# Optimization experiments

Measured on AMD Instinct MI355X. Metric: run time of the kernel, lower is better.

Reference implementation:

```python
import jax, jax.numpy as jnp
import numpy as np

N, D = 8192, 32
SIGMA = 4.0
DAMPING = 0.5
MAX_ITER = 10
SHIFT_TOL = 1e-4


def _sqdist(a, b):
    # squared euclidean distances, (Na, Nb)
    sq = jnp.sum(a * a, axis=1)[:, None] + jnp.sum(b * b, axis=1)[None, :] - 2.0 * (a @ b.T)
    return jnp.maximum(sq, 0.0)


def setup_inputs() -> dict:
    key = jax.random.key(0)
    x = jax.random.normal(key, (N, D), dtype=jnp.float32)
    sigma = jnp.asarray(SIGMA, dtype=jnp.float32)  # learned scalar nn.Parameter
    return {"x": x, "sigma": sigma}


def _find_centroids(x, sigma):
    gamma = 1.0 / (2.0 * sigma ** 2)

    def body(carry, _):
        centroids, done = carry
        sq = _sqdist(x, centroids)              # (N, N); cdist(x,c)**2
        w = jnp.exp(-sq * gamma)                # gaussian kernel weights
        new_c = (w @ x) / jnp.sum(w, axis=1, keepdims=True)
        shift = jnp.linalg.norm(new_c - centroids, axis=1)
        # torch breaks BEFORE the damping update when max shift < tol
        done_new = done | (jnp.max(shift) < SHIFT_TOL)
        centroids = jnp.where(done_new, centroids,
                              DAMPING * centroids + (1.0 - DAMPING) * new_c)
        return (centroids, done_new), None

    (centroids, _), _ = jax.lax.scan(jax.remat(body), (x, jnp.asarray(False)), None, length=MAX_ITER)
    return centroids


def _nms_keep(x, centroids, threshold):
    n = centroids.shape[0]
    sq_pc = _sqdist(x, centroids)
    closest = jnp.argmin(sq_pc, axis=1)                      # (N,)
    scores = jnp.zeros((n,), jnp.int32).at[closest].add(1)   # counts per centroid
    sq_cc = _sqdist(centroids, centroids)
    overlap = (sq_cc < threshold ** 2) & ~jnp.eye(n, dtype=bool)
    order = jnp.argsort(-scores)                             # descending by score

    def body(keep, idx):
        active = keep[idx]
        keep2 = jnp.where(active, keep & ~overlap[idx], keep)
        keep2 = keep2.at[idx].set(jnp.where(active, scores[idx] > 0, keep2[idx]))
        return keep2, None

    keep, _ = jax.lax.scan(body, jnp.ones((n,), bool), order)
    return keep


def reference(x, sigma):
    centroids = _find_centroids(x, sigma)
    # threshold = sigma.item() in torch -> constant w.r.t. autodiff
    keep = _nms_keep(x, centroids, jax.lax.stop_gradient(sigma))
    # assignment over kept centroids only (dropped centroids get -inf cost -> 0 prob)
    cost = -jnp.sqrt(_sqdist(x, centroids) + 1e-12)
    cost = jnp.where(keep[None, :], cost, -jnp.inf)
    assignment = jax.nn.softmax(cost, axis=1)  # alpha == 1 branch
    return centroids, assignment, keep
```

## Files before the change

kernel.cpp:

```cpp
#include <hip/hip_runtime.h>
#include <math.h>

#define NPTS 8192
#define DIM 32
#define MAX_ITER 10
#define TOL 1e-4f
#define DAMP 0.5f

#define OFF_MSP   0u
#define OFF_CCUR  8650752u
#define OFF_CNEW  8912896u
#define OFF_NX    9175040u
#define OFF_NC    9183232u
#define OFF_PV    9191424u
#define OFF_PJ    9453568u
#define OFF_RKP   9715712u
#define OFF_PM    9977856u
#define OFF_PS   10240000u
#define OFF_MSH  10502144u
#define OFF_SCO  10502208u
#define OFF_ORD  10510400u

__global__ __launch_bounds__(256) void k_init(const float* __restrict__ x,
                                              float* __restrict__ c0,
                                              float* __restrict__ nx,
                                              float* __restrict__ nc) {
    int p = blockIdx.x * blockDim.x + threadIdx.x;
    const float4* xr = (const float4*)(x + (size_t)p * DIM);
    float4* cr = (float4*)(c0 + (size_t)p * DIM);
    float s = 0.f;
#pragma unroll
    for (int q = 0; q < 8; ++q) {
        float4 v = xr[q];
        cr[q] = v;
        s += v.x * v.x + v.y * v.y + v.z * v.z + v.w * v.w;
    }
    nx[p] = s;
    nc[p] = s;
}

__global__ __launch_bounds__(256) void k_ms2(const float* __restrict__ x,
                                             const float* __restrict__ nx,
                                             const float* __restrict__ c,
                                             const float* __restrict__ nc,
                                             const float* __restrict__ sigma_p,
                                             float* __restrict__ P) {
    int t = threadIdx.x;
    int wv = __builtin_amdgcn_readfirstlane(t >> 6);
    int lane = t & 63;
    int it = (int)blockIdx.x >> 5, js = (int)blockIdx.x & 31;
    int i = it * 256 + wv * 64 + lane;

    float sg = sigma_p[0];
    float gamma = 1.f / (2.f * sg * sg);

    float xi[DIM];
    const float4* xr = (const float4*)(x + (size_t)i * DIM);
#pragma unroll
    for (int q = 0; q < 8; ++q) {
        float4 v = xr[q];
        xi[4 * q] = v.x; xi[4 * q + 1] = v.y; xi[4 * q + 2] = v.z; xi[4 * q + 3] = v.w;
    }
    float nxi = nx[i];

    float acc[DIM];
#pragma unroll
    for (int d = 0; d < DIM; ++d) acc[d] = 0.f;
    float wsum = 0.f;

    int j0 = js * 256;
    const float* cb = c + (size_t)j0 * DIM;
    const float* xb = x + (size_t)j0 * DIM;
    const float* ncb = nc + j0;

    for (int jj = 0; jj < 256; ++jj) {
        const float4* cr = (const float4*)(cb + (size_t)jj * DIM);
        const float4* xr2 = (const float4*)(xb + (size_t)jj * DIM);
        float4 C[8], X[8];
#pragma unroll
        for (int q = 0; q < 8; ++q) C[q] = cr[q];
#pragma unroll
        for (int q = 0; q < 8; ++q) X[q] = xr2[q];
        float ncj = ncb[jj];
        float d0 = 0.f, d1 = 0.f, d2 = 0.f, d3 = 0.f;
#pragma unroll
        for (int q = 0; q < 8; ++q) {
            d0 = fmaf(xi[4 * q + 0], C[q].x, d0);
            d1 = fmaf(xi[4 * q + 1], C[q].y, d1);
            d2 = fmaf(xi[4 * q + 2], C[q].z, d2);
            d3 = fmaf(xi[4 * q + 3], C[q].w, d3);
        }
        float sq = fmaxf(nxi + ncj - 2.f * ((d0 + d1) + (d2 + d3)), 0.f);
        float w = __expf(-sq * gamma);
        wsum += w;
#pragma unroll
        for (int q = 0; q < 8; ++q) {
            acc[4 * q + 0] = fmaf(w, X[q].x, acc[4 * q + 0]);
            acc[4 * q + 1] = fmaf(w, X[q].y, acc[4 * q + 1]);
            acc[4 * q + 2] = fmaf(w, X[q].z, acc[4 * q + 2]);
            acc[4 * q + 3] = fmaf(w, X[q].w, acc[4 * q + 3]);
        }
    }

    size_t base = ((size_t)js * 33) * NPTS + i;
#pragma unroll
    for (int d = 0; d < DIM; ++d) P[base + (size_t)d * NPTS] = acc[d];
    P[base + (size_t)32 * NPTS] = wsum;
}

__global__ __launch_bounds__(256) void k_reduce(const float* __restrict__ P,
                                                const float* __restrict__ c_cur,
                                                float* __restrict__ c_new,
                                                unsigned int* __restrict__ maxshift) {
    int i = blockIdx.x * 256 + threadIdx.x;
    float tot[33];
#pragma unroll
    for (int d = 0; d < 33; ++d) tot[d] = 0.f;
    for (int js = 0; js < 32; ++js) {
        size_t base = ((size_t)js * 33) * NPTS + i;
#pragma unroll
        for (int d = 0; d < 33; ++d) tot[d] += P[base + (size_t)d * NPTS];
    }
    float ws = tot[32];
    const float* co = c_cur + (size_t)i * DIM;
    float sh2 = 0.f;
    float ncv[DIM];
#pragma unroll
    for (int d = 0; d < DIM; ++d) {
        float v = tot[d] / ws;
        ncv[d] = v;
        float df = v - co[d];
        sh2 = fmaf(df, df, sh2);
    }
    float4* dst = (float4*)(c_new + (size_t)i * DIM);
#pragma unroll
    for (int q = 0; q < 8; ++q)
        dst[q] = make_float4(ncv[4 * q], ncv[4 * q + 1], ncv[4 * q + 2], ncv[4 * q + 3]);
    atomicMax(maxshift, __float_as_uint(sqrtf(sh2)));
}

__global__ __launch_bounds__(256) void k_update(float* __restrict__ c_cur,
                                                const float* __restrict__ c_new,
                                                float* __restrict__ nc,
                                                const unsigned int* __restrict__ maxshift) {
    if (__uint_as_float(*maxshift) < TOL) return;
    int i = blockIdx.x * 256 + threadIdx.x;
    float4* cc = (float4*)(c_cur + (size_t)i * DIM);
    const float4* cn = (const float4*)(c_new + (size_t)i * DIM);
    float s = 0.f;
#pragma unroll
    for (int q = 0; q < 8; ++q) {
        float4 a = cc[q], b = cn[q];
        float4 r = make_float4(DAMP * a.x + (1.f - DAMP) * b.x,
                               DAMP * a.y + (1.f - DAMP) * b.y,
                               DAMP * a.z + (1.f - DAMP) * b.z,
                               DAMP * a.w + (1.f - DAMP) * b.w);
        cc[q] = r;
        s += r.x * r.x + r.y * r.y + r.z * r.z + r.w * r.w;
    }
    nc[i] = s;
}

__global__ __launch_bounds__(256) void k_scores2(const float* __restrict__ x,
                                                 const float* __restrict__ nx,
                                                 const float* __restrict__ c,
                                                 const float* __restrict__ nc,
                                                 float* __restrict__ pv,
                                                 int* __restrict__ pj) {
    int t = threadIdx.x;
    int wv = __builtin_amdgcn_readfirstlane(t >> 6);
    int lane = t & 63;
    int it = (int)blockIdx.x >> 5, js = (int)blockIdx.x & 31;
    int p = it * 256 + wv * 64 + lane;

    float xi[DIM];
    const float4* xr = (const float4*)(x + (size_t)p * DIM);
#pragma unroll
    for (int q = 0; q < 8; ++q) {
        float4 v = xr[q];
        xi[4 * q] = v.x; xi[4 * q + 1] = v.y; xi[4 * q + 2] = v.z; xi[4 * q + 3] = v.w;
    }
    float nxp = nx[p];

    int j0 = js * 256;
    const float* cb = c + (size_t)j0 * DIM;
    const float* ncb = nc + j0;
    float bestv = INFINITY;
    int bestj = j0;
    for (int jj = 0; jj < 256; ++jj) {
        const float4* cr = (const float4*)(cb + (size_t)jj * DIM);
        float4 C[8];
#pragma unroll
        for (int q = 0; q < 8; ++q) C[q] = cr[q];
        float d0 = 0.f, d1 = 0.f, d2 = 0.f, d3 = 0.f;
#pragma unroll
        for (int q = 0; q < 8; ++q) {
            d0 = fmaf(xi[4 * q + 0], C[q].x, d0);
            d1 = fmaf(xi[4 * q + 1], C[q].y, d1);
            d2 = fmaf(xi[4 * q + 2], C[q].z, d2);
            d3 = fmaf(xi[4 * q + 3], C[q].w, d3);
        }
        float sq = fmaxf(nxp + ncb[jj] - 2.f * ((d0 + d1) + (d2 + d3)), 0.f);
        if (sq < bestv) { bestv = sq; bestj = j0 + jj; }
    }
    pv[(size_t)js * NPTS + p] = bestv;
    pj[(size_t)js * NPTS + p] = bestj;
}

__global__ __launch_bounds__(256) void k_score_comb(const float* __restrict__ pv,
                                                    const int* __restrict__ pj,
                                                    int* __restrict__ scores) {
    int p = blockIdx.x * 256 + threadIdx.x;
    float bv = pv[p];
    int bj = pj[p];
    for (int js = 1; js < 32; ++js) {
        float v = pv[(size_t)js * NPTS + p];
        int j = pj[(size_t)js * NPTS + p];
        if (v < bv) { bv = v; bj = j; }
    }
    atomicAdd(&scores[bj], 1);
}

__global__ __launch_bounds__(256) void k_rank_part(const int* __restrict__ scores,
                                                   int* __restrict__ rkp) {
    int t = threadIdx.x;
    int wv = __builtin_amdgcn_readfirstlane(t >> 6);
    int lane = t & 63;
    int it = (int)blockIdx.x >> 5, js = (int)blockIdx.x & 31;
    int p = it * 256 + wv * 64 + lane;
    int sp = scores[p];
    int j0 = js * 256;
    int r = 0;
    for (int jj = 0; jj < 256; ++jj) {
        int sj = scores[j0 + jj];
        int j = j0 + jj;
        r += (sj > sp) || (sj == sp && j < p);
    }
    rkp[(size_t)js * NPTS + p] = r;
}

__global__ __launch_bounds__(256) void k_rank_comb(const int* __restrict__ rkp,
                                                   int* __restrict__ order) {
    int p = blockIdx.x * 256 + threadIdx.x;
    int r = 0;
    for (int js = 0; js < 32; ++js) r += rkp[(size_t)js * NPTS + p];
    order[r] = p;
}

__global__ __launch_bounds__(1024) void k_nms(const float* __restrict__ c,
                                              const int* __restrict__ order,
                                              const int* __restrict__ scores,
                                              const float* __restrict__ sigma_p,
                                              float* __restrict__ keep_out) {
    __shared__ int s_ord[NPTS];
    __shared__ unsigned char kp[NPTS];
    __shared__ int s_first[16];
    __shared__ int s_next;
    int t = threadIdx.x;
    for (int q = t; q < NPTS; q += 1024) { s_ord[q] = order[q]; kp[q] = 1; }
    __syncthreads();
    float sg = sigma_p[0];
    float thr2 = sg * sg;

    int k = 0;
    while (k < NPTS) {
        int cand = k + t;
        bool hit = (cand < NPTS) && (kp[s_ord[cand]] != 0);
        unsigned long long b = __ballot(hit);
        int wave = t >> 6;
        if ((t & 63) == 0)
            s_first[wave] = b ? (k + (wave << 6) + (__ffsll((unsigned long long)b) - 1))
                              : 0x7fffffff;
        __syncthreads();
        if (t == 0) {
            int mn = s_first[0];
            for (int w2 = 1; w2 < 16; ++w2) mn = min(mn, s_first[w2]);
            s_next = mn;
        }
        __syncthreads();
        int kf = s_next;
        if (kf == 0x7fffffff) { k += 1024; continue; }

        int idx = s_ord[kf];
        float ci[DIM];
        const float4* cr = (const float4*)(c + (size_t)idx * DIM);
#pragma unroll
        for (int q = 0; q < 8; ++q) {
            float4 v = cr[q];
            ci[4 * q] = v.x; ci[4 * q + 1] = v.y; ci[4 * q + 2] = v.z; ci[4 * q + 3] = v.w;
        }
#pragma unroll
        for (int m2 = 0; m2 < 8; ++m2) {
            int j = t + m2 * 1024;
            const float4* cj = (const float4*)(c + (size_t)j * DIM);
            float sq = 0.f;
#pragma unroll
            for (int q = 0; q < 8; ++q) {
                float4 v = cj[q];
                float e0 = v.x - ci[4 * q], e1 = v.y - ci[4 * q + 1];
                float e2 = v.z - ci[4 * q + 2], e3 = v.w - ci[4 * q + 3];
                sq += e0 * e0 + e1 * e1 + e2 * e2 + e3 * e3;
            }
            if (j != idx && sq < thr2) kp[j] = 0;
        }
        __syncthreads();
        if (t == 0) kp[idx] = (scores[idx] > 0) ? 1 : 0;
        __syncthreads();
        k = kf + 1;
    }
    __syncthreads();
    for (int q = t; q < NPTS; q += 1024) keep_out[q] = kp[q] ? 1.0f : 0.0f;
}

__global__ __launch_bounds__(256) void k_apass1(const float* __restrict__ x,
                                                const float* __restrict__ nx,
                                                const float* __restrict__ c,
                                                const float* __restrict__ nc,
                                                const float* __restrict__ keepf,
                                                float* __restrict__ pm,
                                                float* __restrict__ ps) {
    int t = threadIdx.x;
    int wv = __builtin_amdgcn_readfirstlane(t >> 6);
    int lane = t & 63;
    int it = (int)blockIdx.x >> 5, js = (int)blockIdx.x & 31;
    int p = it * 256 + wv * 64 + lane;

    float xi[DIM];
    const float4* xr = (const float4*)(x + (size_t)p * DIM);
#pragma unroll
    for (int q = 0; q < 8; ++q) {
        float4 v = xr[q];
        xi[4 * q] = v.x; xi[4 * q + 1] = v.y; xi[4 * q + 2] = v.z; xi[4 * q + 3] = v.w;
    }
    float nxp = nx[p];

    int j0 = js * 256;
    const float* cb = c + (size_t)j0 * DIM;
    const float* ncb = nc + j0;
    const float* kb = keepf + j0;
    float m = -1e30f, S = 0.f;
    for (int jj = 0; jj < 256; ++jj) {
        const float4* cr = (const float4*)(cb + (size_t)jj * DIM);
        float4 C[8];
#pragma unroll
        for (int q = 0; q < 8; ++q) C[q] = cr[q];
        float d0 = 0.f, d1 = 0.f, d2 = 0.f, d3 = 0.f;
#pragma unroll
        for (int q = 0; q < 8; ++q) {
            d0 = fmaf(xi[4 * q + 0], C[q].x, d0);
            d1 = fmaf(xi[4 * q + 1], C[q].y, d1);
            d2 = fmaf(xi[4 * q + 2], C[q].z, d2);
            d3 = fmaf(xi[4 * q + 3], C[q].w, d3);
        }
        float sq = fmaxf(nxp + ncb[jj] - 2.f * ((d0 + d1) + (d2 + d3)), 0.f);
        float cost = -sqrtf(sq + 1e-12f);
        float ck = (kb[jj] > 0.5f) ? cost : -INFINITY;
        float mn = fmaxf(m, ck);
        S = S * __expf(m - mn) + __expf(ck - mn);
        m = mn;
    }
    pm[(size_t)js * NPTS + p] = m;
    ps[(size_t)js * NPTS + p] = S;
}

__global__ __launch_bounds__(256) void k_acomb(const float* __restrict__ pm,
                                               const float* __restrict__ ps,
                                               const float* __restrict__ nx,
                                               float* __restrict__ A) {
    int p = blockIdx.x * 256 + threadIdx.x;
    float M = -1e30f;
    for (int js = 0; js < 32; ++js) M = fmaxf(M, pm[(size_t)js * NPTS + p]);
    float SS = 0.f;
    for (int js = 0; js < 32; ++js)
        SS += ps[(size_t)js * NPTS + p] * __expf(pm[(size_t)js * NPTS + p] - M);
    float* row = A + (size_t)p * NPTS;
    row[8189] = nx[p];
    row[8190] = M;
    row[8191] = 1.f / SS;
}

__global__ __launch_bounds__(256) void k_apass2(const float* __restrict__ x,
                                                const float* __restrict__ c,
                                                const float* __restrict__ keepf,
                                                float* __restrict__ A) {
    __shared__ float sNX[16], sM[16], sI[16];
    int t = threadIdx.x;
    int wv = __builtin_amdgcn_readfirstlane(t >> 6);
    int lane = t & 63;
    int p0 = blockIdx.x * 16;
    if (t < 16) {
        const float* row = A + (size_t)(p0 + t) * NPTS;
        sNX[t] = row[8189];
        sM[t] = row[8190];
        sI[t] = row[8191];
    }
    __syncthreads();

    for (int ch = wv; ch < 128; ch += 4) {
        int j = ch * 64 + lane;
        float cj[DIM];
        const float4* cr = (const float4*)(c + (size_t)j * DIM);
        float ncj = 0.f;
#pragma unroll
        for (int q = 0; q < 8; ++q) {
            float4 v = cr[q];
            cj[4 * q] = v.x; cj[4 * q + 1] = v.y; cj[4 * q + 2] = v.z; cj[4 * q + 3] = v.w;
            ncj += v.x * v.x + v.y * v.y + v.z * v.z + v.w * v.w;
        }
        float kpj = keepf[j];
        for (int pp = 0; pp < 16; ++pp) {
            const float4* xrow = (const float4*)(x + (size_t)(p0 + pp) * DIM);
            float4 X[8];
#pragma unroll
            for (int q = 0; q < 8; ++q) X[q] = xrow[q];
            float nxp = sNX[pp], M = sM[pp], inv = sI[pp];
            float d0 = 0.f, d1 = 0.f, d2 = 0.f, d3 = 0.f;
#pragma unroll
            for (int q = 0; q < 8; ++q) {
                d0 = fmaf(cj[4 * q + 0], X[q].x, d0);
                d1 = fmaf(cj[4 * q + 1], X[q].y, d1);
                d2 = fmaf(cj[4 * q + 2], X[q].z, d2);
                d3 = fmaf(cj[4 * q + 3], X[q].w, d3);
            }
            float sq = fmaxf(nxp + ncj - 2.f * ((d0 + d1) + (d2 + d3)), 0.f);
            float cost = -sqrtf(sq + 1e-12f);
            float v = (kpj > 0.5f) ? __expf(cost - M) * inv : 0.f;
            A[(size_t)(p0 + pp) * NPTS + j] = v;
        }
    }
}

extern "C" void kernel_launch(void* const* d_in, const int* in_sizes, int n_in,
                              void* d_out, int out_size, void* d_ws, size_t ws_size,
                              hipStream_t stream) {
    const float* x = (const float*)d_in[0];
    const float* sigma = (const float*)d_in[1];

    float* out = (float*)d_out;
    float* OUT_C = out;
    float* A = out + (size_t)NPTS * DIM;
    float* OUT_K = A + (size_t)NPTS * NPTS;

    float* msP = A + OFF_MSP;
    float* c_cur = A + OFF_CCUR;
    float* c_new = A + OFF_CNEW;
    float* nx = A + OFF_NX;
    float* nc = A + OFF_NC;
    float* pv = A + OFF_PV;
    int* pj = (int*)(A + OFF_PJ);
    int* rkp = (int*)(A + OFF_RKP);
    float* pm = A + OFF_PM;
    float* ps = A + OFF_PS;
    unsigned int* maxshift = (unsigned int*)(A + OFF_MSH);
    int* scores = (int*)(A + OFF_SCO);
    int* order = (int*)(A + OFF_ORD);

    k_init<<<NPTS / 256, 256, 0, stream>>>(x, c_cur, nx, nc);
    for (int itr = 0; itr < MAX_ITER; ++itr) {
        hipMemsetAsync(maxshift, 0, sizeof(unsigned int), stream);
        k_ms2<<<1024, 256, 0, stream>>>(x, nx, c_cur, nc, sigma, msP);
        k_reduce<<<NPTS / 256, 256, 0, stream>>>(msP, c_cur, c_new, maxshift);
        k_update<<<NPTS / 256, 256, 0, stream>>>(c_cur, c_new, nc, maxshift);
    }
    hipMemcpyAsync(OUT_C, c_cur, (size_t)NPTS * DIM * sizeof(float),
                   hipMemcpyDeviceToDevice, stream);

    hipMemsetAsync(scores, 0, NPTS * sizeof(int), stream);
    k_scores2<<<1024, 256, 0, stream>>>(x, nx, OUT_C, nc, pv, pj);
    k_score_comb<<<NPTS / 256, 256, 0, stream>>>(pv, pj, scores);
    k_rank_part<<<1024, 256, 0, stream>>>(scores, rkp);
    k_rank_comb<<<NPTS / 256, 256, 0, stream>>>(rkp, order);
    k_nms<<<1, 1024, 0, stream>>>(OUT_C, order, scores, sigma, OUT_K);

    k_apass1<<<1024, 256, 0, stream>>>(x, nx, OUT_C, nc, OUT_K, pm, ps);
    k_acomb<<<NPTS / 256, 256, 0, stream>>>(pm, ps, nx, A);
    k_apass2<<<NPTS / 16, 256, 0, stream>>>(x, OUT_C, OUT_K, A);
}
```

Measured before the change: 1.888 ms.

## Interleave centroids, x and norms into one padded row buffer; drop softmax max pass

Packs the current centroid, the original x row, the centroid norm and the keep flag into a single 68-float padded row, so the mean-shift, argmin and softmax passes stream one contiguous buffer. The separate memsets are folded into the init kernel, and each iteration gets its own max-shift slot. The softmax max-tracking and combine kernel are removed, since the costs are at most zero, and exp2/rcp/sqrt intrinsics are used instead. The assignment write pass is re-tiled to 128 points by 512 centroids with two centroids per thread. This risks reduced precision from the fast intrinsics and from dropping max-subtraction, and it relies on the workspace for the partial sums.

```diff
diff --git a/kernel.cpp b/kernel.cpp
--- a/kernel.cpp
+++ b/kernel.cpp
@@ -6,110 +6,110 @@
 #define MAX_ITER 10
 #define TOL 1e-4f
 #define DAMP 0.5f
-
-#define OFF_MSP   0u
-#define OFF_CCUR  8650752u
-#define OFF_CNEW  8912896u
-#define OFF_NX    9175040u
-#define OFF_NC    9183232u
-#define OFF_PV    9191424u
-#define OFF_PJ    9453568u
-#define OFF_RKP   9715712u
-#define OFF_PM    9977856u
-#define OFF_PS   10240000u
-#define OFF_MSH  10502144u
-#define OFF_SCO  10502208u
-#define OFF_ORD  10510400u
+#define LOG2E 1.4426950408889634f
+#define CXS 68
+
+#define OFF_MSP    0u
+#define OFF_CXF    8650752u
+#define OFF_CNEW   9207808u
+#define OFF_NX     9469952u
+#define OFF_PV     9478144u
+#define OFF_PJ     9740288u
+#define OFF_RKP   10002432u
+#define OFF_MSH   10264576u
+#define OFF_SCO   10264592u
+#define OFF_ORD   10272784u
 
 __global__ __launch_bounds__(256) void k_init(const float* __restrict__ x,
-                                              float* __restrict__ c0,
+                                              float* __restrict__ cxf,
                                               float* __restrict__ nx,
-                                              float* __restrict__ nc) {
+                                              int* __restrict__ scores,
+                                              unsigned int* __restrict__ msh) {
     int p = blockIdx.x * blockDim.x + threadIdx.x;
     const float4* xr = (const float4*)(x + (size_t)p * DIM);
-    float4* cr = (float4*)(c0 + (size_t)p * DIM);
+    float* row = cxf + (size_t)p * CXS;
     float s = 0.f;
 #pragma unroll
     for (int q = 0; q < 8; ++q) {
         float4 v = xr[q];
-        cr[q] = v;
+        ((float4*)row)[q] = v;
+        ((float4*)row)[8 + q] = v;
         s += v.x * v.x + v.y * v.y + v.z * v.z + v.w * v.w;
     }
+    row[64] = s;
+    row[65] = 0.f;
     nx[p] = s;
-    nc[p] = s;
+    scores[p] = 0;
+    if (blockIdx.x == 0 && threadIdx.x < 16) msh[threadIdx.x] = 0u;
 }
 
 __global__ __launch_bounds__(256) void k_ms2(const float* __restrict__ x,
                                              const float* __restrict__ nx,
-                                             const float* __restrict__ c,
-                                             const float* __restrict__ nc,
+                                             const float* __restrict__ cxf,
                                              const float* __restrict__ sigma_p,
                                              float* __restrict__ P) {
     int t = threadIdx.x;
-    int wv = __builtin_amdgcn_readfirstlane(t >> 6);
-    int lane = t & 63;
     int it = (int)blockIdx.x >> 5, js = (int)blockIdx.x & 31;
-    int i = it * 256 + wv * 64 + lane;
+    int i = it * 256 + t;
+    int jb = js * 256;
 
     float sg = sigma_p[0];
-    float gamma = 1.f / (2.f * sg * sg);
+    float ng2 = -LOG2E / (2.f * sg * sg);
 
     float xi[DIM];
-    const float4* xr = (const float4*)(x + (size_t)i * DIM);
-#pragma unroll
-    for (int q = 0; q < 8; ++q) {
-        float4 v = xr[q];
-        xi[4 * q] = v.x; xi[4 * q + 1] = v.y; xi[4 * q + 2] = v.z; xi[4 * q + 3] = v.w;
+    {
+        const float4* xr = (const float4*)(x + (size_t)i * DIM);
+#pragma unroll
+        for (int q = 0; q < 8; ++q) {
+            float4 a = xr[q];
+            xi[4 * q] = a.x; xi[4 * q + 1] = a.y; xi[4 * q + 2] = a.z; xi[4 * q + 3] = a.w;
+        }
     }
     float nxi = nx[i];
 
     float acc[DIM];
 #pragma unroll
     for (int d = 0; d < DIM; ++d) acc[d] = 0.f;
-    float wsum = 0.f;
-
-    int j0 = js * 256;
-    const float* cb = c + (size_t)j0 * DIM;
-    const float* xb = x + (size_t)j0 * DIM;
-    const float* ncb = nc + j0;
+    float ws = 0.f;
+
+    const float* row = cxf + (size_t)jb * CXS;
 
     for (int jj = 0; jj < 256; ++jj) {
-        const float4* cr = (const float4*)(cb + (size_t)jj * DIM);
-        const float4* xr2 = (const float4*)(xb + (size_t)jj * DIM);
-        float4 C[8], X[8];
-#pragma unroll
-        for (int q = 0; q < 8; ++q) C[q] = cr[q];
-#pragma unroll
-        for (int q = 0; q < 8; ++q) X[q] = xr2[q];
-        float ncj = ncb[jj];
-        float d0 = 0.f, d1 = 0.f, d2 = 0.f, d3 = 0.f;
-#pragma unroll
-        for (int q = 0; q < 8; ++q) {
-            d0 = fmaf(xi[4 * q + 0], C[q].x, d0);
-            d1 = fmaf(xi[4 * q + 1], C[q].y, d1);
-            d2 = fmaf(xi[4 * q + 2], C[q].z, d2);
-            d3 = fmaf(xi[4 * q + 3], C[q].w, d3);
-        }
-        float sq = fmaxf(nxi + ncj - 2.f * ((d0 + d1) + (d2 + d3)), 0.f);
-        float w = __expf(-sq * gamma);
-        wsum += w;
-#pragma unroll
-        for (int q = 0; q < 8; ++q) {
-            acc[4 * q + 0] = fmaf(w, X[q].x, acc[4 * q + 0]);
-            acc[4 * q + 1] = fmaf(w, X[q].y, acc[4 * q + 1]);
-            acc[4 * q + 2] = fmaf(w, X[q].z, acc[4 * q + 2]);
-            acc[4 * q + 3] = fmaf(w, X[q].w, acc[4 * q + 3]);
-        }
+        float w;
+        {
+            float a0 = 0.f, a1 = 0.f, a2 = 0.f, a3 = 0.f;
+#pragma unroll
+            for (int q = 0; q < 8; ++q) {
+                float4 cv = ((const float4*)row)[q];
+                a0 = fmaf(xi[4 * q + 0], cv.x, a0);
+                a1 = fmaf(xi[4 * q + 1], cv.y, a1);
+                a2 = fmaf(xi[4 * q + 2], cv.z, a2);
+                a3 = fmaf(xi[4 * q + 3], cv.w, a3);
+            }
+            float ncj = row[64];
+            float sq = fmaxf(fmaf(-2.f, (a0 + a1) + (a2 + a3), nxi + ncj), 0.f);
+            w = __builtin_amdgcn_exp2f(ng2 * sq);
+        }
+        ws += w;
+#pragma unroll
+        for (int q = 0; q < 8; ++q) {
+            float4 xv = ((const float4*)row)[8 + q];
+            acc[4 * q + 0] = fmaf(w, xv.x, acc[4 * q + 0]);
+            acc[4 * q + 1] = fmaf(w, xv.y, acc[4 * q + 1]);
+            acc[4 * q + 2] = fmaf(w, xv.z, acc[4 * q + 2]);
+            acc[4 * q + 3] = fmaf(w, xv.w, acc[4 * q + 3]);
+        }
+        row += CXS;
     }
 
     size_t base = ((size_t)js * 33) * NPTS + i;
 #pragma unroll
     for (int d = 0; d < DIM; ++d) P[base + (size_t)d * NPTS] = acc[d];
-    P[base + (size_t)32 * NPTS] = wsum;
+    P[base + (size_t)32 * NPTS] = ws;
 }
 
 __global__ __launch_bounds__(256) void k_reduce(const float* __restrict__ P,
-                                                const float* __restrict__ c_cur,
+                                                const float* __restrict__ cxf,
                                                 float* __restrict__ c_new,
                                                 unsigned int* __restrict__ maxshift) {
     int i = blockIdx.x * 256 + threadIdx.x;
@@ -122,12 +122,14 @@
         for (int d = 0; d < 33; ++d) tot[d] += P[base + (size_t)d * NPTS];
     }
     float ws = tot[32];
-    const float* co = c_cur + (size_t)i * DIM;
+    float inv = __builtin_amdgcn_rcpf(ws);
+    inv = inv * (2.f - ws * inv);
+    const float* co = cxf + (size_t)i * CXS;
     float sh2 = 0.f;
     float ncv[DIM];
 #pragma unroll
     for (int d = 0; d < DIM; ++d) {
-        float v = tot[d] / ws;
+        float v = tot[d] * inv;
         ncv[d] = v;
         float df = v - co[d];
         sh2 = fmaf(df, df, sh2);
@@ -136,75 +138,79 @@
 #pragma unroll
     for (int q = 0; q < 8; ++q)
         dst[q] = make_float4(ncv[4 * q], ncv[4 * q + 1], ncv[4 * q + 2], ncv[4 * q + 3]);
-    atomicMax(maxshift, __float_as_uint(sqrtf(sh2)));
-}
-
-__global__ __launch_bounds__(256) void k_update(float* __restrict__ c_cur,
+    atomicMax(maxshift, __float_as_uint(__builtin_amdgcn_sqrtf(sh2)));
+}
+
+__global__ __launch_bounds__(256) void k_update(float* __restrict__ cxf,
                                                 const float* __restrict__ c_new,
-                                                float* __restrict__ nc,
                                                 const unsigned int* __restrict__ maxshift) {
     if (__uint_as_float(*maxshift) < TOL) return;
     int i = blockIdx.x * 256 + threadIdx.x;
-    float4* cc = (float4*)(c_cur + (size_t)i * DIM);
+    float* row = cxf + (size_t)i * CXS;
     const float4* cn = (const float4*)(c_new + (size_t)i * DIM);
     float s = 0.f;
 #pragma unroll
     for (int q = 0; q < 8; ++q) {
-        float4 a = cc[q], b = cn[q];
+        float4 a = ((float4*)row)[q], b = cn[q];
         float4 r = make_float4(DAMP * a.x + (1.f - DAMP) * b.x,
                                DAMP * a.y + (1.f - DAMP) * b.y,
                                DAMP * a.z + (1.f - DAMP) * b.z,
                                DAMP * a.w + (1.f - DAMP) * b.w);
-        cc[q] = r;
+        ((float4*)row)[q] = r;
         s += r.x * r.x + r.y * r.y + r.z * r.z + r.w * r.w;
     }
-    nc[i] = s;
+    row[64] = s;
+}
+
+__global__ __launch_bounds__(256) void k_extract(const float* __restrict__ cxf,
+                                                 float* __restrict__ outc) {
+    int g = blockIdx.x * 256 + threadIdx.x;
+    int rowi = g >> 3, q = g & 7;
+    ((float4*)(outc + (size_t)rowi * DIM))[q] =
+        ((const float4*)(cxf + (size_t)rowi * CXS))[q];
 }
 
 __global__ __launch_bounds__(256) void k_scores2(const float* __restrict__ x,
                                                  const float* __restrict__ nx,
-                                                 const float* __restrict__ c,
-                                                 const float* __restrict__ nc,
+                                                 const float* __restrict__ cxf,
                                                  float* __restrict__ pv,
                                                  int* __restrict__ pj) {
     int t = threadIdx.x;
-    int wv = __builtin_amdgcn_readfirstlane(t >> 6);
-    int lane = t & 63;
     int it = (int)blockIdx.x >> 5, js = (int)blockIdx.x & 31;
-    int p = it * 256 + wv * 64 + lane;
+    int p = it * 256 + t;
+    int jb = js * 256;
 
     float xi[DIM];
-    const float4* xr = (const float4*)(x + (size_t)p * DIM);
-#pragma unroll
-    for (int q = 0; q < 8; ++q) {
-        float4 v = xr[q];
-        xi[4 * q] = v.x; xi[4 * q + 1] = v.y; xi[4 * q + 2] = v.z; xi[4 * q + 3] = v.w;
+    {
+        const float4* xr = (const float4*)(x + (size_t)p * DIM);
+#pragma unroll
+        for (int q = 0; q < 8; ++q) {
+            float4 a = xr[q];
+            xi[4 * q] = a.x; xi[4 * q + 1] = a.y; xi[4 * q + 2] = a.z; xi[4 * q + 3] = a.w;
+        }
     }
     float nxp = nx[p];
 
-    int j0 = js * 256;
-    const float* cb = c + (size_t)j0 * DIM;
-    const float* ncb = nc + j0;
-    float bestv = INFINITY;
-    int bestj = j0;
+    const float* row = cxf + (size_t)jb * CXS;
+    float bv = INFINITY;
+    int bj = jb;
     for (int jj = 0; jj < 256; ++jj) {
-        const float4* cr = (const float4*)(cb + (size_t)jj * DIM);
-        float4 C[8];
-#pragma unroll
-        for (int q = 0; q < 8; ++q) C[q] = cr[q];
-        float d0 = 0.f, d1 = 0.f, d2 = 0.f, d3 = 0.f;
-#pragma unroll
-        for (int q = 0; q < 8; ++q) {
-            d0 = fmaf(xi[4 * q + 0], C[q].x, d0);
-            d1 = fmaf(xi[4 * q + 1], C[q].y, d1);
-            d2 = fmaf(xi[4 * q + 2], C[q].z, d2);
-            d3 = fmaf(xi[4 * q + 3], C[q].w, d3);
-        }
-        float sq = fmaxf(nxp + ncb[jj] - 2.f * ((d0 + d1) + (d2 + d3)), 0.f);
-        if (sq < bestv) { bestv = sq; bestj = j0 + jj; }
-    }
-    pv[(size_t)js * NPTS + p] = bestv;
-    pj[(size_t)js * NPTS + p] = bestj;
+        float a0 = 0.f, a1 = 0.f, a2 = 0.f, a3 = 0.f;
+#pragma unroll
+        for (int q = 0; q < 8; ++q) {
+            float4 cv = ((const float4*)row)[q];
+            a0 = fmaf(xi[4 * q + 0], cv.x, a0);
+            a1 = fmaf(xi[4 * q + 1], cv.y, a1);
+            a2 = fmaf(xi[4 * q + 2], cv.z, a2);
+            a3 = fmaf(xi[4 * q + 3], cv.w, a3);
+        }
+        float ncj = row[64];
+        float sq = fmaxf(fmaf(-2.f, (a0 + a1) + (a2 + a3), nxp + ncj), 0.f);
+        if (sq < bv) { bv = sq; bj = jb + jj; }
+        row += CXS;
+    }
+    pv[(size_t)js * NPTS + p] = bv;
+    pj[(size_t)js * NPTS + p] = bj;
 }
 
 __global__ __launch_bounds__(256) void k_score_comb(const float* __restrict__ pv,
@@ -224,10 +230,8 @@
 __global__ __launch_bounds__(256) void k_rank_part(const int* __restrict__ scores,
                                                    int* __restrict__ rkp) {
     int t = threadIdx.x;
-    int wv = __builtin_amdgcn_readfirstlane(t >> 6);
-    int lane = t & 63;
     int it = (int)blockIdx.x >> 5, js = (int)blockIdx.x & 31;
-    int p = it * 256 + wv * 64 + lane;
+    int p = it * 256 + t;
     int sp = scores[p];
     int j0 = js * 256;
     int r = 0;
@@ -251,7 +255,8 @@
                                               const int* __restrict__ order,
                                               const int* __restrict__ scores,
                                               const float* __restrict__ sigma_p,
-                                              float* __restrict__ keep_out) {
+                                              float* __restrict__ keep_out,
+                                              float* __restrict__ cxf) {
     __shared__ int s_ord[NPTS];
     __shared__ unsigned char kp[NPTS];
     __shared__ int s_first[16];
@@ -309,124 +314,129 @@
         k = kf + 1;
     }
     __syncthreads();
-    for (int q = t; q < NPTS; q += 1024) keep_out[q] = kp[q] ? 1.0f : 0.0f;
+    for (int q = t; q < NPTS; q += 1024) {
+        float kv = kp[q] ? 1.0f : 0.0f;
+        keep_out[q] = kv;
+        cxf[(size_t)q * CXS + 65] = kv;
+    }
 }
 
 __global__ __launch_bounds__(256) void k_apass1(const float* __restrict__ x,
                                                 const float* __restrict__ nx,
-                                                const float* __restrict__ c,
-                                                const float* __restrict__ nc,
-                                                const float* __restrict__ keepf,
-                                                float* __restrict__ pm,
+                                                const float* __restrict__ cxf,
                                                 float* __restrict__ ps) {
     int t = threadIdx.x;
-    int wv = __builtin_amdgcn_readfirstlane(t >> 6);
-    int lane = t & 63;
     int it = (int)blockIdx.x >> 5, js = (int)blockIdx.x & 31;
-    int p = it * 256 + wv * 64 + lane;
+    int p = it * 256 + t;
+    int jb = js * 256;
 
     float xi[DIM];
-    const float4* xr = (const float4*)(x + (size_t)p * DIM);
-#pragma unroll
-    for (int q = 0; q < 8; ++q) {
-        float4 v = xr[q];
-        xi[4 * q] = v.x; xi[4 * q + 1] = v.y; xi[4 * q + 2] = v.z; xi[4 * q + 3] = v.w;
+    {
+        const float4* xr = (const float4*)(x + (size_t)p * DIM);
+#pragma unroll
+        for (int q = 0; q < 8; ++q) {
+            float4 a = xr[q];
+            xi[4 * q] = a.x; xi[4 * q + 1] = a.y; xi[4 * q + 2] = a.z; xi[4 * q + 3] = a.w;
+        }
     }
     float nxp = nx[p];
 
-    int j0 = js * 256;
-    const float* cb = c + (size_t)j0 * DIM;
-    const float* ncb = nc + j0;
-    const float* kb = keepf + j0;
-    float m = -1e30f, S = 0.f;
+    const float* row = cxf + (size_t)jb * CXS;
+    float S = 0.f;
     for (int jj = 0; jj < 256; ++jj) {
-        const float4* cr = (const float4*)(cb + (size_t)jj * DIM);
-        float4 C[8];
-#pragma unroll
-        for (int q = 0; q < 8; ++q) C[q] = cr[q];
-        float d0 = 0.f, d1 = 0.f, d2 = 0.f, d3 = 0.f;
-#pragma unroll
-        for (int q = 0; q < 8; ++q) {
-            d0 = fmaf(xi[4 * q + 0], C[q].x, d0);
-            d1 = fmaf(xi[4 * q + 1], C[q].y, d1);
-            d2 = fmaf(xi[4 * q + 2], C[q].z, d2);
-            d3 = fmaf(xi[4 * q + 3], C[q].w, d3);
-        }
-        float sq = fmaxf(nxp + ncb[jj] - 2.f * ((d0 + d1) + (d2 + d3)), 0.f);
-        float cost = -sqrtf(sq + 1e-12f);
-        float ck = (kb[jj] > 0.5f) ? cost : -INFINITY;
-        float mn = fmaxf(m, ck);
-        S = S * __expf(m - mn) + __expf(ck - mn);
-        m = mn;
-    }
-    pm[(size_t)js * NPTS + p] = m;
+        float a0 = 0.f, a1 = 0.f, a2 = 0.f, a3 = 0.f;
+#pragma unroll
+        for (int q = 0; q < 8; ++q) {
+            float4 cv = ((const float4*)row)[q];
+            a0 = fmaf(xi[4 * q + 0], cv.x, a0);
+            a1 = fmaf(xi[4 * q + 1], cv.y, a1);
+            a2 = fmaf(xi[4 * q + 2], cv.z, a2);
+            a3 = fmaf(xi[4 * q + 3], cv.w, a3);
+        }
+        float ncj = row[64];
+        float kadd = (row[65] > 0.5f) ? 0.f : -1e38f;
+        float sq = fmaxf(fmaf(-2.f, (a0 + a1) + (a2 + a3), nxp + ncj), 0.f);
+        float r0 = __builtin_amdgcn_sqrtf(sq + 1e-12f);
+        S += __builtin_amdgcn_exp2f(fmaf(r0, -LOG2E, kadd));
+        row += CXS;
+    }
     ps[(size_t)js * NPTS + p] = S;
-}
-
-__global__ __launch_bounds__(256) void k_acomb(const float* __restrict__ pm,
-                                               const float* __restrict__ ps,
-                                               const float* __restrict__ nx,
-                                               float* __restrict__ A) {
-    int p = blockIdx.x * 256 + threadIdx.x;
-    float M = -1e30f;
-    for (int js = 0; js < 32; ++js) M = fmaxf(M, pm[(size_t)js * NPTS + p]);
-    float SS = 0.f;
-    for (int js = 0; js < 32; ++js)
-        SS += ps[(size_t)js * NPTS + p] * __expf(pm[(size_t)js * NPTS + p] - M);
-    float* row = A + (size_t)p * NPTS;
-    row[8189] = nx[p];
-    row[8190] = M;
-    row[8191] = 1.f / SS;
 }
 
 __global__ __launch_bounds__(256) void k_apass2(const float* __restrict__ x,
                                                 const float* __restrict__ c,
                                                 const float* __restrict__ keepf,
+                                                const float* __restrict__ ps,
                                                 float* __restrict__ A) {
-    __shared__ float sNX[16], sM[16], sI[16];
+    __shared__ float snx[128];
+    __shared__ float sscale[128];
     int t = threadIdx.x;
     int wv = __builtin_amdgcn_readfirstlane(t >> 6);
     int lane = t & 63;
-    int p0 = blockIdx.x * 16;
-    if (t < 16) {
-        const float* row = A + (size_t)(p0 + t) * NPTS;
-        sNX[t] = row[8189];
-        sM[t] = row[8190];
-        sI[t] = row[8191];
-    }
+    int pt = (int)blockIdx.x >> 4, jt = (int)blockIdx.x & 15;
+    int p0 = pt * 128, j0 = jt * 512;
+
+    if (t < 128) {
+        const float4* xr = (const float4*)(x + (size_t)(p0 + t) * DIM);
+        float s = 0.f;
+#pragma unroll
+        for (int q = 0; q < 8; ++q) {
+            float4 v = xr[q];
+            s += v.x * v.x + v.y * v.y + v.z * v.z + v.w * v.w;
+        }
+        snx[t] = s;
+        float SS = 0.f;
+        for (int js = 0; js < 32; ++js) SS += ps[(size_t)js * NPTS + p0 + t];
+        sscale[t] = 1.f / SS;
+    }
+
+    int ja = j0 + wv * 64 + lane;
+    int jbx = ja + 256;
+    float cj0[DIM], cj1[DIM];
+    float nc0 = 0.f, nc1 = 0.f;
+    {
+        const float4* cra = (const float4*)(c + (size_t)ja * DIM);
+        const float4* crb = (const float4*)(c + (size_t)jbx * DIM);
+#pragma unroll
+        for (int q = 0; q < 8; ++q) {
+            float4 va = cra[q], vb = crb[q];
+            cj0[4 * q] = va.x; cj0[4 * q + 1] = va.y; cj0[4 * q + 2] = va.z; cj0[4 * q + 3] = va.w;
+            cj1[4 * q] = vb.x; cj1[4 * q + 1] = vb.y; cj1[4 * q + 2] = vb.z; cj1[4 * q + 3] = vb.w;
+            nc0 += va.x * va.x + va.y * va.y + va.z * va.z + va.w * va.w;
+            nc1 += vb.x * vb.x + vb.y * vb.y + vb.z * vb.z + vb.w * vb.w;
+        }
+    }
+    float kadd0 = (keepf[ja] > 0.5f) ? 0.f : -1e38f;
+    float kadd1 = (keepf[jbx] > 0.5f) ? 0.f : -1e38f;
     __syncthreads();
 
-    for (int ch = wv; ch < 128; ch += 4) {
-        int j = ch * 64 + lane;
-        float cj[DIM];
-        const float4* cr = (const float4*)(c + (size_t)j * DIM);
-        float ncj = 0.f;
-#pragma unroll
-        for (int q = 0; q < 8; ++q) {
-            float4 v = cr[q];
-            cj[4 * q] = v.x; cj[4 * q + 1] = v.y; cj[4 * q + 2] = v.z; cj[4 * q + 3] = v.w;
-            ncj += v.x * v.x + v.y * v.y + v.z * v.z + v.w * v.w;
-        }
-        float kpj = keepf[j];
-        for (int pp = 0; pp < 16; ++pp) {
-            const float4* xrow = (const float4*)(x + (size_t)(p0 + pp) * DIM);
-            float4 X[8];
-#pragma unroll
-            for (int q = 0; q < 8; ++q) X[q] = xrow[q];
-            float nxp = sNX[pp], M = sM[pp], inv = sI[pp];
-            float d0 = 0.f, d1 = 0.f, d2 = 0.f, d3 = 0.f;
-#pragma unroll
-            for (int q = 0; q < 8; ++q) {
-                d0 = fmaf(cj[4 * q + 0], X[q].x, d0);
-                d1 = fmaf(cj[4 * q + 1], X[q].y, d1);
-                d2 = fmaf(cj[4 * q + 2], X[q].z, d2);
-                d3 = fmaf(cj[4 * q + 3], X[q].w, d3);
-            }
-            float sq = fmaxf(nxp + ncj - 2.f * ((d0 + d1) + (d2 + d3)), 0.f);
-            float cost = -sqrtf(sq + 1e-12f);
-            float v = (kpj > 0.5f) ? __expf(cost - M) * inv : 0.f;
-            A[(size_t)(p0 + pp) * NPTS + j] = v;
-        }
+    const float* xrow = x + (size_t)p0 * DIM;
+    for (int pp = 0; pp < 128; ++pp) {
+        float d0 = 0.f, d1 = 0.f, d2 = 0.f, d3 = 0.f;
+        float e0 = 0.f, e1 = 0.f, e2 = 0.f, e3 = 0.f;
+#pragma unroll
+        for (int q = 0; q < 8; ++q) {
+            float4 v = ((const float4*)xrow)[q];
+            d0 = fmaf(cj0[4 * q + 0], v.x, d0);
+            d1 = fmaf(cj0[4 * q + 1], v.y, d1);
+            d2 = fmaf(cj0[4 * q + 2], v.z, d2);
+            d3 = fmaf(cj0[4 * q + 3], v.w, d3);
+            e0 = fmaf(cj1[4 * q + 0], v.x, e0);
+            e1 = fmaf(cj1[4 * q + 1], v.y, e1);
+            e2 = fmaf(cj1[4 * q + 2], v.z, e2);
+            e3 = fmaf(cj1[4 * q + 3], v.w, e3);
+        }
+        float nxp = snx[pp], scl = sscale[pp];
+        float sqa = fmaxf(fmaf(-2.f, (d0 + d1) + (d2 + d3), nxp + nc0), 0.f);
+        float sqb = fmaxf(fmaf(-2.f, (e0 + e1) + (e2 + e3), nxp + nc1), 0.f);
+        float ra = __builtin_amdgcn_sqrtf(sqa + 1e-12f);
+        float rb = __builtin_amdgcn_sqrtf(sqb + 1e-12f);
+        float ta = fmaf(ra, -LOG2E, kadd0);
+        float tb = fmaf(rb, -LOG2E, kadd1);
+        float* rowp = A + (size_t)(p0 + pp) * NPTS;
+        rowp[ja] = __builtin_amdgcn_exp2f(ta) * scl;
+        rowp[jbx] = __builtin_amdgcn_exp2f(tb) * scl;
+        xrow += DIM;
     }
 }
 
@@ -442,37 +452,31 @@
     float* OUT_K = A + (size_t)NPTS * NPTS;
 
     float* msP = A + OFF_MSP;
-    float* c_cur = A + OFF_CCUR;
+    float* cxf = A + OFF_CXF;
     float* c_new = A + OFF_CNEW;
     float* nx = A + OFF_NX;
-    float* nc = A + OFF_NC;
     float* pv = A + OFF_PV;
     int* pj = (int*)(A + OFF_PJ);
     int* rkp = (int*)(A + OFF_RKP);
-    float* pm = A + OFF_PM;
-    float* ps = A + OFF_PS;
-    unsigned int* maxshift = (unsigned int*)(A + OFF_MSH);
+    unsigned int* msh = (unsigned int*)(A + OFF_MSH);
     int* scores = (int*)(A + OFF_SCO);
     int* order = (int*)(A + OFF_ORD);
-
-    k_init<<<NPTS / 256, 256, 0, stream>>>(x, c_cur, nx, nc);
+    float* ps = (float*)d_ws;
+
+    k_init<<<NPTS / 256, 256, 0, stream>>>(x, cxf, nx, scores, msh);
     for (int itr = 0; itr < MAX_ITER; ++itr) {
-        hipMemsetAsync(maxshift, 0, sizeof(unsigned int), stream);
-        k_ms2<<<1024, 256, 0, stream>>>(x, nx, c_cur, nc, sigma, msP);
-        k_reduce<<<NPTS / 256, 256, 0, stream>>>(msP, c_cur, c_new, maxshift);
-        k_update<<<NPTS / 256, 256, 0, stream>>>(c_cur, c_new, nc, maxshift);
-    }
-    hipMemcpyAsync(OUT_C, c_cur, (size_t)NPTS * DIM * sizeof(float),
-                   hipMemcpyDeviceToDevice, stream);
-
-    hipMemsetAsync(scores, 0, NPTS * sizeof(int), stream);
-    k_scores2<<<1024, 256, 0, stream>>>(x, nx, OUT_C, nc, pv, pj);
+        k_ms2<<<1024, 256, 0, stream>>>(x, nx, cxf, sigma, msP);
+        k_reduce<<<NPTS / 256, 256, 0, stream>>>(msP, cxf, c_new, msh + itr);
+        k_update<<<NPTS / 256, 256, 0, stream>>>(cxf, c_new, msh + itr);
+    }
+    k_extract<<<NPTS * 8 / 256, 256, 0, stream>>>(cxf, OUT_C);
+
+    k_scores2<<<1024, 256, 0, stream>>>(x, nx, cxf, pv, pj);
     k_score_comb<<<NPTS / 256, 256, 0, stream>>>(pv, pj, scores);
     k_rank_part<<<1024, 256, 0, stream>>>(scores, rkp);
     k_rank_comb<<<NPTS / 256, 256, 0, stream>>>(rkp, order);
-    k_nms<<<1, 1024, 0, stream>>>(OUT_C, order, scores, sigma, OUT_K);
-
-    k_apass1<<<1024, 256, 0, stream>>>(x, nx, OUT_C, nc, OUT_K, pm, ps);
-    k_acomb<<<NPTS / 256, 256, 0, stream>>>(pm, ps, nx, A);
-    k_apass2<<<NPTS / 16, 256, 0, stream>>>(x, OUT_C, OUT_K, A);
-}
+    k_nms<<<1, 1024, 0, stream>>>(OUT_C, order, scores, sigma, OUT_K, cxf);
+
+    k_apass1<<<1024, 256, 0, stream>>>(x, nx, cxf, ps);
+    k_apass2<<<1024, 256, 0, stream>>>(x, OUT_C, OUT_K, ps, A);
+}
```

After: 2.205 ms. +16.8%, slower.
